# Kernel tuning notes

Hardware: AMD Instinct MI355X
Metric: run time of the kernel (lower is better)

Reference implementation:

```python
import jax, jax.numpy as jnp
import numpy as np

B, S, D, H = 2, 2048, 2048, 16
HD = D // H            # 128
HALF = HD // 2         # 64
SOFTCAP = 50.0
ROPE_BASE = 10000.0


def setup_inputs() -> dict:
    key = jax.random.key(0)
    k1, k2, k3 = jax.random.split(key, 3)
    inputs = jax.random.normal(k1, (B, S, D), dtype=jnp.float32)
    # param init ~ nnx.initializers.normal() (stddev 0.01 default; scale to keep activations sane)
    w_in = jax.random.normal(k2, (D, H, 3 * HD), dtype=jnp.float32) * (1.0 / np.sqrt(D))
    w_out = jax.random.normal(k3, (H, HD, D), dtype=jnp.float32) * (1.0 / np.sqrt(D))
    # RoPE tables: [S, HALF]
    pos = jnp.arange(S, dtype=jnp.float32)[:, None]
    inv_freq = 1.0 / (ROPE_BASE ** (jnp.arange(HALF, dtype=jnp.float32) / HALF))
    ang = pos * inv_freq[None, :]
    rope_sin = jnp.sin(ang)
    rope_cos = jnp.cos(ang)
    # causal mask [1, 1, S, S]
    mask = jnp.tril(jnp.ones((S, S), dtype=bool))[None, None, :, :]
    return {"inputs": inputs, "w_in": w_in, "w_out": w_out,
            "rope_sin": rope_sin, "rope_cos": rope_cos, "mask": mask}


def apply_rope(x, sin, cos):
    # x: [B, S, H, HD]; sin/cos: [S, HALF] -> broadcast [1, S, 1, HALF]
    sin = sin[None, :, None, :]
    cos = cos[None, :, None, :]
    x1, x2 = x[..., :HALF], x[..., HALF:]
    return jnp.concatenate([x1 * cos - x2 * sin, x2 * cos + x1 * sin], axis=-1)


def reference(inputs, w_in, w_out, rope_sin, rope_cos, mask):
    dtype = inputs.dtype
    # fused QKV projection: [B, S, H, 3*HD]
    qkv = jnp.einsum('bsd,bhf->bshf'.replace('bhf', 'dhf'), inputs, w_in)
    q, k, v = jnp.split(qkv, 3, axis=-1)           # each [B, S, H, HD]
    q = apply_rope(q, rope_sin, rope_cos)
    k = apply_rope(k, rope_sin, rope_cos)
    q = q / jnp.sqrt(jnp.asarray(HD, dtype))
    scores = jnp.einsum('bqhd,bkhd->bhqk', q, k)   # [B, H, S, S]
    big_neg = jnp.finfo(dtype).min
    scores = jnp.where(mask, scores, big_neg)
    scores = jnp.tanh(scores / SOFTCAP) * SOFTCAP  # softcap
    attn = jax.nn.softmax(scores, axis=-1)
    x = jnp.einsum('bhqk,bkhd->bqhd', attn, v)     # [B, S, H, HD]
    out = jnp.einsum('bqhd,hdm->bqm', x, w_out)    # [B, S, D]
    return out
```

## Files before the change

kernel.cpp:

```cpp
#include <hip/hip_runtime.h>

#define B_ 2
#define S_ 2048
#define D_ 2048
#define H_ 16
#define HD_ 128
#define NT_ (S_ / 64)
#define NBUF 6

typedef unsigned short u16;
typedef __bf16 bf16x8 __attribute__((ext_vector_type(8)));
typedef float f32x4 __attribute__((ext_vector_type(4)));

__device__ __forceinline__ float bf2f(u16 u) {
  unsigned int x = ((unsigned int)u) << 16;
  return __builtin_bit_cast(float, x);
}
__device__ __forceinline__ u16 f2bf(float f) {
  unsigned int u = __builtin_bit_cast(unsigned int, f);
  u += 0x7fffu + ((u >> 16) & 1u);
  return (u16)(u >> 16);
}
__device__ __forceinline__ void async16(const void* g, void* l) {
  __builtin_amdgcn_global_load_lds((const __attribute__((address_space(1))) void*)g,
                                   (__attribute__((address_space(3))) void*)l, 16, 0, 0);
}
__device__ __forceinline__ float vexp2(float x) {
  float r;
  asm("v_exp_f32 %0, %1" : "=v"(r) : "v"(x));
  return r;
}
__device__ __forceinline__ float vrcp(float x) {
  float r;
  asm("v_rcp_f32 %0, %1" : "=v"(r) : "v"(x));
  return r;
}

__global__ __launch_bounds__(256) void conv_f32_bf16(const float* __restrict__ in,
                                                     u16* __restrict__ outp, int n) {
  int idx = (blockIdx.x * 256 + threadIdx.x) * 4;
  int stride = gridDim.x * 256 * 4;
  for (; idx < n; idx += stride) {
    float4 v = *(const float4*)(in + idx);
    ushort4 ov = make_ushort4(f2bf(v.x), f2bf(v.y), f2bf(v.z), f2bf(v.w));
    *(ushort4*)(outp + idx) = ov;
  }
}

__global__ __launch_bounds__(256) void transpose_conv(const float* __restrict__ in,
                                                      u16* __restrict__ outp, int R, int C) {
  __shared__ float tile[32][33];
  int c0 = blockIdx.x * 32, r0 = blockIdx.y * 32;
  int tx = threadIdx.x & 31, ty = threadIdx.x >> 5;
#pragma unroll
  for (int yy = 0; yy < 32; yy += 8)
    tile[ty + yy][tx] = in[(size_t)(r0 + ty + yy) * C + c0 + tx];
  __syncthreads();
#pragma unroll
  for (int yy = 0; yy < 32; yy += 8)
    outp[(size_t)(c0 + ty + yy) * R + r0 + tx] = f2bf(tile[tx][ty + yy]);
}

__global__ __launch_bounds__(256) void transpose_v(const u16* __restrict__ in,
                                                   u16* __restrict__ outp) {
  __shared__ u16 tile[32][33];
  int bhh = blockIdx.z;
  const u16* ip = in + (size_t)bhh * S_ * HD_;
  u16* op = outp + (size_t)bhh * HD_ * S_;
  int hd0 = blockIdx.x * 32, s0 = blockIdx.y * 32;
  int tx = threadIdx.x & 31, ty = threadIdx.x >> 5;
#pragma unroll
  for (int yy = 0; yy < 32; yy += 8)
    tile[ty + yy][tx] = ip[(size_t)(s0 + ty + yy) * HD_ + hd0 + tx];
  __syncthreads();
#pragma unroll
  for (int yy = 0; yy < 32; yy += 8)
    op[(size_t)(hd0 + ty + yy) * S_ + s0 + tx] = tile[tx][ty + yy];
}

__global__ __launch_bounds__(256) void rope_kernel(u16* __restrict__ Q, u16* __restrict__ Kk,
                                                   const float* __restrict__ rsin,
                                                   const float* __restrict__ rcos) {
  int t = blockIdx.x * 256 + threadIdx.x;
  u16* base = blockIdx.y ? Kk : Q;
  float scale = blockIdx.y ? 1.0f : 0.08838834764831845f;
  int row = t >> 3, seg = t & 7;
  int s = row & (S_ - 1);
  int i0 = seg * 8;
  u16* p = base + (size_t)row * HD_;
  alignas(16) u16 x1[8], x2[8], o1[8], o2[8];
  *(uint4*)x1 = *(const uint4*)(p + i0);
  *(uint4*)x2 = *(const uint4*)(p + 64 + i0);
  alignas(16) float sn[8], cs[8];
  *(float4*)sn = *(const float4*)(rsin + s * 64 + i0);
  *(float4*)(sn + 4) = *(const float4*)(rsin + s * 64 + i0 + 4);
  *(float4*)cs = *(const float4*)(rcos + s * 64 + i0);
  *(float4*)(cs + 4) = *(const float4*)(rcos + s * 64 + i0 + 4);
#pragma unroll
  for (int j = 0; j < 8; ++j) {
    float a = bf2f(x1[j]), bb = bf2f(x2[j]);
    o1[j] = f2bf((a * cs[j] - bb * sn[j]) * scale);
    o2[j] = f2bf((bb * cs[j] + a * sn[j]) * scale);
  }
  *(uint4*)(p + i0) = *(uint4*)o1;
  *(uint4*)(p + 64 + i0) = *(uint4*)o2;
}

template <int EPI>
__global__ __launch_bounds__(512, 1) void gemm8p(const u16* __restrict__ A,
                                                 const u16* __restrict__ Bt,
                                                 float* __restrict__ C, int K, int N, int gx,
                                                 u16* __restrict__ Qo, u16* __restrict__ Ko,
                                                 u16* __restrict__ Vo) {
  __shared__ alignas(16) u16 lsA[NBUF][256 * 32];
  __shared__ alignas(16) u16 lsB[NBUF][128 * 32];
  const int tid = threadIdx.x;
  const int lane = tid & 63;
  const int wid = tid >> 6;
  const int g = lane >> 4, lr = lane & 15;
  const int wm = wid >> 1, wn = wid & 1;

  const int nwg = gx << 4;
  const int bid = blockIdx.x;
  const int swz = (bid & 7) * (nwg >> 3) + (bid >> 3);
  const int m_idx = swz & 15, n_idx = swz >> 4;
  const size_t m0 = (size_t)m_idx * 256, n0 = (size_t)n_idx * 128;

  const int la0 = tid, la1 = 512 + tid;
  const int rowA0 = la0 >> 2, slA0 = la0 & 3;
  const int rowA1 = la1 >> 2, slA1 = la1 & 3;
  const int rowB = tid >> 2, slB = tid & 3;
  const u16* srcA0 = A + (m0 + rowA0) * K + ((slA0 ^ ((rowA0 >> 1) & 3)) << 3);
  const u16* srcA1 = A + (m0 + rowA1) * K + ((slA1 ^ ((rowA1 >> 1) & 3)) << 3);
  const u16* srcB = Bt + (n0 + rowB) * K + ((slB ^ ((rowB >> 1) & 3)) << 3);

#define STAGE(t, bufi)                                          \
  {                                                             \
    const int koff = (t) << 5;                                  \
    async16(srcA0 + koff, (char*)lsA[bufi] + la0 * 16);         \
    async16(srcA1 + koff, (char*)lsA[bufi] + la1 * 16);         \
    async16(srcB + koff, (char*)lsB[bufi] + tid * 16);          \
  }

  int ofsA[4], ofsB[4];
#pragma unroll
  for (int i = 0; i < 4; ++i) {
    int ra = wm * 64 + i * 16 + lr;
    ofsA[i] = ra * 64 + ((g ^ ((ra >> 1) & 3)) << 4);
    int rb = wn * 64 + i * 16 + lr;
    ofsB[i] = rb * 64 + ((g ^ ((rb >> 1) & 3)) << 4);
  }

  f32x4 acc[4][4] = {};
  const int nk = K >> 5;

#pragma unroll
  for (int t = 0; t < NBUF - 1; ++t) STAGE(t, t);
  asm volatile("s_waitcnt vmcnt(12)" ::: "memory");
  __builtin_amdgcn_s_barrier();

  int buf = 0;
#pragma unroll 1
  for (int kt = 0; kt < nk; ++kt) {
    bf16x8 af[4], bfr[4];
#pragma unroll
    for (int i = 0; i < 4; ++i) af[i] = *(const bf16x8*)((const char*)lsA[buf] + ofsA[i]);
#pragma unroll
    for (int j = 0; j < 4; ++j) bfr[j] = *(const bf16x8*)((const char*)lsB[buf] + ofsB[j]);
    const int st = kt + NBUF - 1;
    const int sbuf = buf == 0 ? NBUF - 1 : buf - 1;
    if (st < nk) STAGE(st, sbuf);
    __builtin_amdgcn_s_barrier();
    __builtin_amdgcn_s_setprio(1);
#pragma unroll
    for (int i = 0; i < 4; ++i)
#pragma unroll
      for (int j = 0; j < 4; ++j)
        acc[i][j] = __builtin_amdgcn_mfma_f32_16x16x32_bf16(af[i], bfr[j], acc[i][j], 0, 0, 0);
    __builtin_amdgcn_s_setprio(0);
    asm volatile("s_waitcnt vmcnt(12)" ::: "memory");
    __builtin_amdgcn_s_barrier();
    buf = buf == NBUF - 1 ? 0 : buf + 1;
  }
#undef STAGE

  if (EPI == 0) {
#pragma unroll
    for (int i = 0; i < 4; ++i)
#pragma unroll
      for (int j = 0; j < 4; ++j)
#pragma unroll
        for (int r = 0; r < 4; ++r) {
          size_t m = m0 + wm * 64 + i * 16 + 4 * g + r;
          size_t n = n0 + wn * 64 + j * 16 + lr;
          C[m * N + n] = acc[i][j][r];
        }
  } else {
    const int part = n_idx % 3, h = n_idx / 3;
    u16* dst = (part == 0) ? Qo : (part == 1 ? Ko : Vo);
#pragma unroll
    for (int i = 0; i < 4; ++i)
#pragma unroll
      for (int j = 0; j < 4; ++j)
#pragma unroll
        for (int r = 0; r < 4; ++r) {
          int m = (int)m0 + wm * 64 + i * 16 + 4 * g + r;
          int hd = wn * 64 + j * 16 + lr;
          int b = m >> 11, s = m & (S_ - 1);
          dst[((size_t)(b * H_ + h) * S_ + s) * HD_ + hd] = f2bf(acc[i][j][r]);
        }
  }
}

__global__ __launch_bounds__(256) void attn_fwd(const u16* __restrict__ Q, const u16* __restrict__ K,
                                                const u16* __restrict__ VT, u16* __restrict__ X) {
  const int bx = blockIdx.x;
  const int bh = blockIdx.y;
  const int tid = threadIdx.x;
  const int lane = tid & 63, wid = tid >> 6;
  const int g = lane >> 4, lr = lane & 15;

  __shared__ alignas(16) u16 lsK[2][64 * 128];
  __shared__ alignas(16) u16 lsV[2][128 * 64];
  __shared__ alignas(16) u16 lsP[4][16 * 72];

  const u16* Qp = Q + (size_t)bh * S_ * HD_;
  const u16* Kp = K + (size_t)bh * S_ * HD_;
  const u16* Vp = VT + (size_t)bh * HD_ * S_;
  u16* myP = lsP[wid];
  const int b = bh >> 4, h = bh & 15;

  const float c1 = -0.057707802f;
  const float c2 = -144.26950409f;

#pragma unroll 1
  for (int pass = 0; pass < 2; ++pass) {
    const int qt = pass ? bx : (NT_ - 1 - bx);
    const int qrow = qt * 64 + wid * 16 + lr;
    const int qbase = qt * 64 + wid * 16 + 4 * g;

    bf16x8 qf[4];
#pragma unroll
    for (int kc = 0; kc < 4; ++kc)
      qf[kc] = *(const bf16x8*)(Qp + (size_t)qrow * HD_ + kc * 32 + g * 8);

    f32x4 o[8] = {};
    float psum[4] = {0.f, 0.f, 0.f, 0.f};

#pragma unroll
    for (int p = 0; p < 4; ++p) {
      int c = p * 256 + tid;
      int rowk = c >> 4;
      int wsk = ((c & 15) << 4) ^ ((rowk & 7) << 4);
      async16((const char*)Kp + (((size_t)rowk) << 8) + wsk, (char*)lsK[0] + c * 16);
      int rowv = c >> 3;
      int wsv = ((c & 7) << 4) ^ ((rowv & 7) << 4);
      async16((const char*)Vp + (size_t)rowv * (S_ * 2) + wsv, (char*)lsV[0] + c * 16);
    }
    __syncthreads();

    int cur = 0;
    for (int kt = 0; kt <= qt; ++kt) {
      if (kt < qt) {
        const int nxt = kt + 1;
#pragma unroll
        for (int p = 0; p < 4; ++p) {
          int c = p * 256 + tid;
          int rowk = c >> 4;
          int wsk = ((c & 15) << 4) ^ ((rowk & 7) << 4);
          async16((const char*)Kp + (((size_t)(nxt * 64 + rowk)) << 8) + wsk,
                  (char*)lsK[cur ^ 1] + c * 16);
          int rowv = c >> 3;
          int wsv = ((c & 7) << 4) ^ ((rowv & 7) << 4);
          async16((const char*)Vp + (size_t)rowv * (S_ * 2) + nxt * 128 + wsv,
                  (char*)lsV[cur ^ 1] + c * 16);
        }
      }
      f32x4 sc[4];
#pragma unroll
      for (int jn = 0; jn < 4; ++jn) {
        f32x4 a = {0.f, 0.f, 0.f, 0.f};
        const int row = jn * 16 + lr;
        const int sw = (row & 7) << 4;
#pragma unroll
        for (int kc = 0; kc < 4; ++kc) {
          int w = (kc * 64 + g * 16) ^ sw;
          bf16x8 kf = *(const bf16x8*)((const char*)lsK[cur] + row * 256 + w);
          a = __builtin_amdgcn_mfma_f32_16x16x32_bf16(qf[kc], kf, a, 0, 0, 0);
        }
        sc[jn] = a;
      }
#pragma unroll
      for (int jn = 0; jn < 4; ++jn) {
        int key = kt * 64 + jn * 16 + lr;
#pragma unroll
        for (int r = 0; r < 4; ++r) {
          float z = vexp2(c1 * sc[jn][r]);
          float p = vexp2(c2 * z * vrcp(1.f + z));
          if (key > qbase + r) p = 0.f;
          psum[r] += p;
          myP[(4 * g + r) * 72 + jn * 16 + lr] = f2bf(p);
        }
      }
#pragma unroll
      for (int kc = 0; kc < 2; ++kc) {
        bf16x8 pa = *(const bf16x8*)(myP + lr * 72 + kc * 32 + g * 8);
#pragma unroll
        for (int jh = 0; jh < 8; ++jh) {
          int row = jh * 16 + lr;
          int w = (kc * 64 + g * 16) ^ ((row & 7) << 4);
          bf16x8 vf = *(const bf16x8*)((const char*)lsV[cur] + row * 128 + w);
          o[jh] = __builtin_amdgcn_mfma_f32_16x16x32_bf16(pa, vf, o[jh], 0, 0, 0);
        }
      }
      __syncthreads();
      cur ^= 1;
    }
    float lsum[4];
#pragma unroll
    for (int r = 0; r < 4; ++r) {
      float s = psum[r];
#pragma unroll
      for (int msk = 1; msk < 16; msk <<= 1) s += __shfl_xor(s, msk, 64);
      lsum[r] = s;
    }
#pragma unroll
    for (int r = 0; r < 4; ++r) {
      float inv = 1.f / lsum[r];
      int s = qbase + r;
      u16* xp = X + ((size_t)(b * S_ + s)) * D_ + h * HD_;
#pragma unroll
      for (int jh = 0; jh < 8; ++jh) xp[jh * 16 + lr] = f2bf(o[jh][r] * inv);
    }
  }
}

extern "C" void kernel_launch(void* const* d_in, const int* in_sizes, int n_in,
                              void* d_out, int out_size, void* d_ws, size_t ws_size,
                              hipStream_t stream) {
  const float* inputs = (const float*)d_in[0];
  const float* w_in = (const float*)d_in[1];
  const float* w_out = (const float*)d_in[2];
  const float* rsin = (const float*)d_in[3];
  const float* rcos = (const float*)d_in[4];
  float* out = (float*)d_out;

  char* ws = (char*)d_ws;
  u16* bfA = (u16*)(ws);
  u16* w_inT = (u16*)(ws + 16777216);
  u16* Qraw = (u16*)(ws + 41943040);
  u16* Kraw = (u16*)(ws + 58720256);
  u16* Vraw = (u16*)(ws + 75497472);
  u16* VT = (u16*)(ws + 92274688);
  u16* Xbuf = (u16*)(ws);
  u16* w_outT = (u16*)(ws + 16777216);

  conv_f32_bf16<<<2048, 256, 0, stream>>>(inputs, bfA, B_ * S_ * D_);
  transpose_conv<<<dim3(6144 / 32, 2048 / 32), 256, 0, stream>>>(w_in, w_inT, 2048, 6144);
  gemm8p<1><<<768, 512, 0, stream>>>(bfA, w_inT, nullptr, 2048, 6144, 48, Qraw, Kraw, Vraw);
  transpose_conv<<<dim3(2048 / 32, 2048 / 32), 256, 0, stream>>>(w_out, w_outT, 2048, 2048);
  rope_kernel<<<dim3(2048, 2), 256, 0, stream>>>(Qraw, Kraw, rsin, rcos);
  transpose_v<<<dim3(4, 64, 32), 256, 0, stream>>>(Vraw, VT);
  attn_fwd<<<dim3(NT_ / 2, 32), 256, 0, stream>>>(Qraw, Kraw, VT, Xbuf);
  gemm8p<0><<<256, 512, 0, stream>>>(Xbuf, w_outT, out, 2048, 2048, 16,
                                     nullptr, nullptr, nullptr);
}
```

Before: 310.3 us.

## Use 256x256 tile GEMM with split B-fragment pipelining for QKV projection

Adds a new gemm256 kernel that computes 256x256 output tiles with 8 waves laid out 2x4, a 4-stage async LDS ring, and a k-step split into two MFMA halves with interleaved loads and barriers. The QKV projection now launches 384 workgroups with this kernel instead of 768 workgroups of the 256x128 kernel. The larger tile raises arithmetic intensity and halves redundant A-tile loads. In exchange it uses 128 accumulator registers per lane, and the 384-block grid may fill the CUs less evenly.

```diff
diff --git a/kernel.cpp b/kernel.cpp
--- a/kernel.cpp
+++ b/kernel.cpp
@@ -107,6 +107,139 @@
 }
 
 template <int EPI>
+__global__ __launch_bounds__(512, 2) void gemm256(const u16* __restrict__ A,
+                                                  const u16* __restrict__ Bt,
+                                                  float* __restrict__ C, int K, int N, int nchunk,
+                                                  u16* __restrict__ Qo, u16* __restrict__ Ko,
+                                                  u16* __restrict__ Vo) {
+  __shared__ alignas(16) u16 lsA[4][256 * 32];
+  __shared__ alignas(16) u16 lsB[4][256 * 32];
+  const int tid = threadIdx.x;
+  const int lane = tid & 63;
+  const int wid = tid >> 6;
+  const int g = lane >> 4, lr = lane & 15;
+  const int wm = wid >> 2, wn = wid & 3;
+
+  const int nwg = nchunk << 4;
+  const int bid = blockIdx.x;
+  const int swz = (bid & 7) * (nwg >> 3) + (bid >> 3);
+  const int m_idx = swz & 15, n_idx = swz >> 4;
+  const size_t m0 = (size_t)m_idx * 256, n0 = (size_t)n_idx * 256;
+
+  const u16* sA[2];
+  const u16* sB[2];
+  int dst16[2];
+#pragma unroll
+  for (int r = 0; r < 2; ++r) {
+    int idx = r * 512 + tid;
+    int row = idx >> 2, sl = idx & 3;
+    int slot = sl ^ ((row >> 1) & 3);
+    sA[r] = A + (m0 + row) * K + (slot << 3);
+    sB[r] = Bt + (n0 + row) * K + (slot << 3);
+    dst16[r] = idx * 16;
+  }
+#define STA(t, bufi)                                            \
+  {                                                             \
+    async16(sA[0] + ((t) << 5), (char*)lsA[bufi] + dst16[0]);   \
+    async16(sA[1] + ((t) << 5), (char*)lsA[bufi] + dst16[1]);   \
+  }
+#define STB(t, bufi)                                            \
+  {                                                             \
+    async16(sB[0] + ((t) << 5), (char*)lsB[bufi] + dst16[0]);   \
+    async16(sB[1] + ((t) << 5), (char*)lsB[bufi] + dst16[1]);   \
+  }
+
+  int ofsA[8], ofsB[4];
+#pragma unroll
+  for (int i = 0; i < 8; ++i) {
+    int ra = wm * 128 + i * 16 + lr;
+    ofsA[i] = ra * 64 + ((g ^ ((ra >> 1) & 3)) << 4);
+  }
+#pragma unroll
+  for (int j = 0; j < 4; ++j) {
+    int rb = wn * 64 + j * 16 + lr;
+    ofsB[j] = rb * 64 + ((g ^ ((rb >> 1) & 3)) << 4);
+  }
+
+  f32x4 acc[8][4] = {};
+  const int nk = K >> 5;
+
+#pragma unroll
+  for (int t = 0; t < 3; ++t) {
+    STA(t, t);
+    STB(t, t);
+  }
+  asm volatile("s_waitcnt vmcnt(8)" ::: "memory");
+  __builtin_amdgcn_s_barrier();
+
+#pragma unroll 1
+  for (int kt = 0; kt < nk; ++kt) {
+    const int buf = kt & 3;
+    const int st = kt + 3;
+    const int sb = st & 3;
+    bf16x8 af[8], bf01[2];
+#pragma unroll
+    for (int i = 0; i < 8; ++i) af[i] = *(const bf16x8*)((const char*)lsA[buf] + ofsA[i]);
+#pragma unroll
+    for (int j = 0; j < 2; ++j) bf01[j] = *(const bf16x8*)((const char*)lsB[buf] + ofsB[j]);
+    if (st < nk) STA(st, sb);
+    __builtin_amdgcn_s_barrier();
+    __builtin_amdgcn_s_setprio(1);
+#pragma unroll
+    for (int i = 0; i < 8; ++i)
+#pragma unroll
+      for (int j = 0; j < 2; ++j)
+        acc[i][j] = __builtin_amdgcn_mfma_f32_16x16x32_bf16(af[i], bf01[j], acc[i][j], 0, 0, 0);
+    __builtin_amdgcn_s_setprio(0);
+    bf16x8 bf23[2];
+#pragma unroll
+    for (int j = 0; j < 2; ++j) bf23[j] = *(const bf16x8*)((const char*)lsB[buf] + ofsB[2 + j]);
+    if (st < nk) STB(st, sb);
+    __builtin_amdgcn_s_barrier();
+    __builtin_amdgcn_s_setprio(1);
+#pragma unroll
+    for (int i = 0; i < 8; ++i)
+#pragma unroll
+      for (int j = 0; j < 2; ++j)
+        acc[i][2 + j] =
+            __builtin_amdgcn_mfma_f32_16x16x32_bf16(af[i], bf23[j], acc[i][2 + j], 0, 0, 0);
+    __builtin_amdgcn_s_setprio(0);
+    asm volatile("s_waitcnt vmcnt(8)" ::: "memory");
+    __builtin_amdgcn_s_barrier();
+  }
+#undef STA
+#undef STB
+
+  if (EPI == 0) {
+#pragma unroll
+    for (int i = 0; i < 8; ++i)
+#pragma unroll
+      for (int j = 0; j < 4; ++j)
+#pragma unroll
+        for (int r = 0; r < 4; ++r) {
+          size_t m = m0 + wm * 128 + i * 16 + 4 * g + r;
+          size_t n = n0 + wn * 64 + j * 16 + lr;
+          C[m * N + n] = acc[i][j][r];
+        }
+  } else {
+    const int c = (int)(n0 >> 7) + (wn >> 1);
+    const int h = c / 3, part = c % 3;
+    u16* dst = (part == 0) ? Qo : (part == 1 ? Ko : Vo);
+#pragma unroll
+    for (int i = 0; i < 8; ++i)
+#pragma unroll
+      for (int j = 0; j < 4; ++j)
+#pragma unroll
+        for (int r = 0; r < 4; ++r) {
+          int m = (int)m0 + wm * 128 + i * 16 + 4 * g + r;
+          int hd = (wn & 1) * 64 + j * 16 + lr;
+          int b = m >> 11, s = m & (S_ - 1);
+          dst[((size_t)(b * H_ + h) * S_ + s) * HD_ + hd] = f2bf(acc[i][j][r]);
+        }
+  }
+}
+
+template <int EPI>
 __global__ __launch_bounds__(512, 1) void gemm8p(const u16* __restrict__ A,
                                                  const u16* __restrict__ Bt,
                                                  float* __restrict__ C, int K, int N, int gx,
@@ -357,7 +490,7 @@
 
   conv_f32_bf16<<<2048, 256, 0, stream>>>(inputs, bfA, B_ * S_ * D_);
   transpose_conv<<<dim3(6144 / 32, 2048 / 32), 256, 0, stream>>>(w_in, w_inT, 2048, 6144);
-  gemm8p<1><<<768, 512, 0, stream>>>(bfA, w_inT, nullptr, 2048, 6144, 48, Qraw, Kraw, Vraw);
+  gemm256<1><<<384, 512, 0, stream>>>(bfA, w_inT, nullptr, 2048, 6144, 24, Qraw, Kraw, Vraw);
   transpose_conv<<<dim3(2048 / 32, 2048 / 32), 256, 0, stream>>>(w_out, w_outT, 2048, 2048);
   rope_kernel<<<dim3(2048, 2), 256, 0, stream>>>(Qraw, Kraw, rsin, rcos);
   transpose_v<<<dim3(4, 64, 32), 256, 0, stream>>>(Vraw, VT);
```

After: 299.4 us. 1.04x faster.

## Use 256x256-tile ping-pong GEMM kernel for fused QKV projection

Applied to the files above, without the earlier changes.

Adds a new GEMM kernel with 256x256 output tiles and a 64-wide K step. It double-buffers LDS in half-tile chunks and interleaves async global-to-LDS loads with MFMA sub-blocks under barriers and s_setprio. The QKV projection now uses it with 384 workgroups instead of 768 smaller ones. The aim is more data reuse per tile and better overlap of loads with compute, at the cost of fewer workgroups (a possible tail effect on 256 CUs) and heavy LDS use.

```diff
diff --git a/kernel.cpp b/kernel.cpp
--- a/kernel.cpp
+++ b/kernel.cpp
@@ -106,6 +106,190 @@
   *(uint4*)(p + 64 + i0) = *(uint4*)o2;
 }
 
+#define BAR __builtin_amdgcn_s_barrier()
+#define LGKM0                                          \
+  {                                                    \
+    asm volatile("s_waitcnt lgkmcnt(0)" ::: "memory"); \
+    __builtin_amdgcn_sched_barrier(0);                 \
+  }
+#define VM4 asm volatile("s_waitcnt vmcnt(4)" ::: "memory")
+#define VM0 asm volatile("s_waitcnt vmcnt(0)" ::: "memory")
+#define P1 __builtin_amdgcn_s_setprio(1)
+#define P0 __builtin_amdgcn_s_setprio(0)
+
+template <int EPI>
+__global__ __launch_bounds__(512, 1) void gemm256_8p(const u16* __restrict__ A,
+                                                     const u16* __restrict__ Bt,
+                                                     float* __restrict__ C, int K, int N,
+                                                     int ntn, u16* __restrict__ Qo,
+                                                     u16* __restrict__ Ko, u16* __restrict__ Vo) {
+  __shared__ alignas(16) u16 lsA[2][256 * 64];
+  __shared__ alignas(16) u16 lsB[2][256 * 64];
+  const int tid = threadIdx.x;
+  const int lane = tid & 63, wid = tid >> 6;
+  const int g = lane >> 4, lr = lane & 15;
+  const int wm = wid >> 2, wn = wid & 3;
+
+  const int nwg = 16 * ntn;
+  const int bid = blockIdx.x;
+  const int swz = (bid & 7) * (nwg >> 3) + (bid >> 3);
+  const int m_idx = swz & 15, n_idx = swz >> 4;
+  const size_t m0 = (size_t)m_idx * 256, n0 = (size_t)n_idx * 256;
+
+  const int row0 = tid >> 3, sl0 = tid & 7;
+  const int row1 = (512 + tid) >> 3, sl1 = tid & 7;
+  const u16* pA0 = A + (m0 + row0) * K + ((sl0 ^ (row0 & 7)) << 3);
+  const u16* pA1 = A + (m0 + row1) * K + ((sl1 ^ (row1 & 7)) << 3);
+  const u16* pB0 = Bt + (n0 + row0) * K + ((sl0 ^ (row0 & 7)) << 3);
+  const u16* pB1 = Bt + (n0 + row1) * K + ((sl1 ^ (row1 & 7)) << 3);
+  const size_t hstep = (size_t)128 * K;
+
+#define STG_A(t, buf, half)                                                                   \
+  {                                                                                           \
+    async16(pA0 + (half) * hstep + (size_t)(t) * 64, (char*)lsA[buf] + (half) * 16384 + tid * 16); \
+    async16(pA1 + (half) * hstep + (size_t)(t) * 64,                                          \
+            (char*)lsA[buf] + (half) * 16384 + 8192 + tid * 16);                              \
+  }
+#define STG_B(t, buf, half)                                                                   \
+  {                                                                                           \
+    async16(pB0 + (half) * hstep + (size_t)(t) * 64, (char*)lsB[buf] + (half) * 16384 + tid * 16); \
+    async16(pB1 + (half) * hstep + (size_t)(t) * 64,                                          \
+            (char*)lsB[buf] + (half) * 16384 + 8192 + tid * 16);                              \
+  }
+
+  const int sw0 = ((g) ^ (lr & 7)) << 4;
+  const int sw1 = ((4 + g) ^ (lr & 7)) << 4;
+
+#define LDA(tb, mh)                                                              \
+  {                                                                              \
+    _Pragma("unroll") for (int i2 = 0; i2 < 4; ++i2) {                           \
+      const char* _p = (const char*)lsA[tb] + (wm * 128 + (mh)*64 + i2 * 16 + lr) * 128; \
+      aF[i2][0] = *(const bf16x8*)(_p + sw0);                                    \
+      aF[i2][1] = *(const bf16x8*)(_p + sw1);                                    \
+    }                                                                            \
+  }
+#define LDB(tb, dst, nh)                                                         \
+  {                                                                              \
+    _Pragma("unroll") for (int j2 = 0; j2 < 2; ++j2) {                           \
+      const char* _p = (const char*)lsB[tb] + (wn * 64 + (nh)*32 + j2 * 16 + lr) * 128; \
+      dst[j2][0] = *(const bf16x8*)(_p + sw0);                                   \
+      dst[j2][1] = *(const bf16x8*)(_p + sw1);                                   \
+    }                                                                            \
+  }
+#define MM(mh, nh, BB)                                                                        \
+  {                                                                                           \
+    _Pragma("unroll") for (int i2 = 0; i2 < 4; ++i2) _Pragma("unroll") for (int j2 = 0;      \
+                                                                            j2 < 2; ++j2) {  \
+      acc[(mh)*4 + i2][(nh)*2 + j2] = __builtin_amdgcn_mfma_f32_16x16x32_bf16(                \
+          aF[i2][0], BB[j2][0], acc[(mh)*4 + i2][(nh)*2 + j2], 0, 0, 0);                      \
+      acc[(mh)*4 + i2][(nh)*2 + j2] = __builtin_amdgcn_mfma_f32_16x16x32_bf16(                \
+          aF[i2][1], BB[j2][1], acc[(mh)*4 + i2][(nh)*2 + j2], 0, 0, 0);                      \
+    }                                                                                         \
+  }
+
+  f32x4 acc[8][4] = {};
+  const int nk2 = K >> 7;
+
+  STG_A(0, 0, 0);
+  STG_B(0, 0, 1);
+  STG_B(0, 0, 0);
+  STG_A(0, 0, 1);
+  STG_A(1, 1, 0);
+  STG_B(1, 1, 1);
+  VM4;
+  BAR;
+
+  bf16x8 aF[4][2], b0[2][2], b1[2][2];
+#pragma unroll 1
+  for (int it = 0; it < nk2 - 1; ++it) {
+    const int t1 = 2 * it + 1, s2 = 2 * it + 2, s3 = 2 * it + 3;
+    LDA(0, 0);
+    LDB(0, b0, 0);
+    STG_B(t1, 1, 0);
+    BAR; LGKM0; P1; MM(0, 0, b0); P0; BAR;
+    LDB(0, b1, 1);
+    STG_A(t1, 1, 1);
+    BAR; LGKM0; P1; MM(0, 1, b1); P0; BAR;
+    LDA(0, 1);
+    STG_A(s2, 0, 0);
+    BAR; LGKM0; P1; MM(1, 1, b1); P0; BAR;
+    STG_B(s2, 0, 1);
+    BAR; LGKM0; P1; MM(1, 0, b0); P0;
+    VM4;
+    BAR;
+    LDA(1, 0);
+    LDB(1, b0, 0);
+    STG_B(s2, 0, 0);
+    BAR; LGKM0; P1; MM(0, 0, b0); P0; BAR;
+    LDB(1, b1, 1);
+    STG_A(s2, 0, 1);
+    BAR; LGKM0; P1; MM(0, 1, b1); P0; BAR;
+    LDA(1, 1);
+    STG_A(s3, 1, 0);
+    BAR; LGKM0; P1; MM(1, 1, b1); P0; BAR;
+    STG_B(s3, 1, 1);
+    BAR; LGKM0; P1; MM(1, 0, b0); P0;
+    VM4;
+    BAR;
+  }
+  {
+    const int t1 = 2 * (nk2 - 1) + 1;
+    LDA(0, 0);
+    LDB(0, b0, 0);
+    STG_B(t1, 1, 0);
+    BAR; LGKM0; P1; MM(0, 0, b0); P0; BAR;
+    LDB(0, b1, 1);
+    STG_A(t1, 1, 1);
+    BAR; LGKM0; P1; MM(0, 1, b1); P0; BAR;
+    LDA(0, 1);
+    BAR; LGKM0; P1; MM(1, 1, b1); P0; BAR;
+    BAR; LGKM0; P1; MM(1, 0, b0); P0;
+    VM0;
+    BAR;
+    LDA(1, 0);
+    LDB(1, b0, 0);
+    BAR; LGKM0; P1; MM(0, 0, b0); P0; BAR;
+    LDB(1, b1, 1);
+    BAR; LGKM0; P1; MM(0, 1, b1); P0; BAR;
+    LDA(1, 1);
+    BAR; LGKM0; P1; MM(1, 1, b1); P0; BAR;
+    BAR; LGKM0; P1; MM(1, 0, b0); P0; BAR;
+  }
+#undef STG_A
+#undef STG_B
+#undef LDA
+#undef LDB
+#undef MM
+
+  if (EPI == 0) {
+#pragma unroll
+    for (int ai = 0; ai < 8; ++ai)
+#pragma unroll
+      for (int bj = 0; bj < 4; ++bj)
+#pragma unroll
+        for (int r = 0; r < 4; ++r) {
+          size_t m = m0 + wm * 128 + (ai >> 2) * 64 + (ai & 3) * 16 + 4 * g + r;
+          size_t n = n0 + wn * 64 + (bj >> 1) * 32 + (bj & 1) * 16 + lr;
+          C[m * N + n] = acc[ai][bj][r];
+        }
+  } else {
+    const int c = (int)(n0 >> 7) + (wn >> 1);
+    const int h = c / 3, part = c % 3;
+    u16* dst = (part == 0) ? Qo : (part == 1 ? Ko : Vo);
+#pragma unroll
+    for (int ai = 0; ai < 8; ++ai)
+#pragma unroll
+      for (int bj = 0; bj < 4; ++bj)
+#pragma unroll
+        for (int r = 0; r < 4; ++r) {
+          int m = (int)m0 + wm * 128 + (ai >> 2) * 64 + (ai & 3) * 16 + 4 * g + r;
+          int hd = (wn & 1) * 64 + (bj >> 1) * 32 + (bj & 1) * 16 + lr;
+          int b = m >> 11, s = m & (S_ - 1);
+          dst[((size_t)(b * H_ + h) * S_ + s) * HD_ + hd] = f2bf(acc[ai][bj][r]);
+        }
+  }
+}
+
 template <int EPI>
 __global__ __launch_bounds__(512, 1) void gemm8p(const u16* __restrict__ A,
                                                  const u16* __restrict__ Bt,
@@ -134,12 +318,12 @@
   const u16* srcA1 = A + (m0 + rowA1) * K + ((slA1 ^ ((rowA1 >> 1) & 3)) << 3);
   const u16* srcB = Bt + (n0 + rowB) * K + ((slB ^ ((rowB >> 1) & 3)) << 3);
 
-#define STAGE(t, bufi)                                          \
-  {                                                             \
-    const int koff = (t) << 5;                                  \
-    async16(srcA0 + koff, (char*)lsA[bufi] + la0 * 16);         \
-    async16(srcA1 + koff, (char*)lsA[bufi] + la1 * 16);         \
-    async16(srcB + koff, (char*)lsB[bufi] + tid * 16);          \
+#define STAGE(t, bufi)                                  \
+  {                                                     \
+    const int koff = (t) << 5;                          \
+    async16(srcA0 + koff, (char*)lsA[bufi] + la0 * 16); \
+    async16(srcA1 + koff, (char*)lsA[bufi] + la1 * 16); \
+    async16(srcB + koff, (char*)lsB[bufi] + tid * 16);  \
   }
 
   int ofsA[4], ofsB[4];
@@ -357,7 +541,8 @@
 
   conv_f32_bf16<<<2048, 256, 0, stream>>>(inputs, bfA, B_ * S_ * D_);
   transpose_conv<<<dim3(6144 / 32, 2048 / 32), 256, 0, stream>>>(w_in, w_inT, 2048, 6144);
-  gemm8p<1><<<768, 512, 0, stream>>>(bfA, w_inT, nullptr, 2048, 6144, 48, Qraw, Kraw, Vraw);
+  gemm256_8p<1><<<384, 512, 0, stream>>>(bfA, w_inT, nullptr, 2048, 6144, 24,
+                                         Qraw, Kraw, Vraw);
   transpose_conv<<<dim3(2048 / 32, 2048 / 32), 256, 0, stream>>>(w_out, w_outT, 2048, 2048);
   rope_kernel<<<dim3(2048, 2), 256, 0, stream>>>(Qraw, Kraw, rsin, rcos);
   transpose_v<<<dim3(4, 64, 32), 256, 0, stream>>>(Vraw, VT);
```

Result: faster. 294.8 us (-5.0%).
